# Kernel optimization log

Measured on AMD Instinct MI355X. Metric: run time of the kernel, lower is better.

## Reference

```python
import jax, jax.numpy as jnp
import numpy as np

EPS = 1e-5

def _ln(x, g, b):
    m = jnp.mean(x, axis=-1, keepdims=True)
    v = jnp.var(x, axis=-1, keepdims=True)
    return (x - m) / jnp.sqrt(v + EPS) * g + b

def _partition(x, nw):
    b, h, w, c = x.shape
    x = x.reshape(b, nw, h // nw, nw, w // nw, c).transpose(0, 1, 3, 2, 4, 5)
    return x.reshape(b * nw * nw, h // nw, w // nw, c)

def _merge(x, nw):
    b_, h, w, c = x.shape
    b = b_ // (nw * nw)
    x = x.reshape(b, nw, nw, h, w, c).transpose(0, 1, 3, 2, 4, 5)
    return x.reshape(b, nw * h, nw * w, c)

def _window_attn(q, k, v, width, height, nw, mask):
    b, _, c = q.shape
    q = q.reshape(b, height, width, c)
    k = k.reshape(b, height, width, c)
    v = v.reshape(b, height, width, c)
    sh, sw = (height // nw) // 2, (width // nw) // 2
    q = jnp.roll(q, (-sh, -sw), (1, 2))
    k = jnp.roll(k, (-sh, -sw), (1, 2))
    v = jnp.roll(v, (-sh, -sw), (1, 2))
    q = _partition(q, nw); k = _partition(k, nw); v = _partition(v, nw)
    N = (height // nw) * (width // nw)
    b_ = b * nw * nw
    qf = q.reshape(b_, N, c); kf = k.reshape(b_, N, c); vf = v.reshape(b_, N, c)
    scale = jnp.asarray(c, qf.dtype) ** 0.5
    scores = jnp.einsum('bnc,bmc->bnm', qf, kf) / scale  # [b_, N, N]
    scores = (scores.reshape(b, nw * nw, N, N) + mask[None]).reshape(b_, N, N)
    attn = jax.nn.softmax(scores, axis=-1)
    out = jnp.einsum('bnm,bmc->bnc', attn, vf)
    out = _merge(out.reshape(b_, height // nw, width // nw, c), nw)
    out = jnp.roll(out, (sh, sw), (1, 2))
    return out.reshape(b, height * width, c)

def _block(feat0, feat1, width, height, mask, nw, wq, wk, wv, wfc, g, be, ffn=None):
    q = feat0 @ wq; k = feat1 @ wk; v = feat1 @ wv
    a = _window_attn(q, k, v, width, height, nw, mask)
    a = _ln(a @ wfc, g, be)
    if ffn is not None:
        w1, w2, fg, fb = ffn
        h = jax.nn.gelu(jnp.concatenate([feat0, a], axis=-1) @ w1, approximate=False)
        a = _ln(h @ w2, fg, fb)
    return feat0 + a

def setup_inputs() -> dict:
    key = jax.random.key(0)
    B, H, W, NW, D = 8, 128, 128, 8, 256
    N = (H // NW) * (W // NW)
    ks = jax.random.split(key, 16)
    s = D ** -0.5
    return {
        'feat0': jax.random.normal(ks[0], (B, H * W, D), jnp.float32),
        'feat1': jax.random.normal(ks[1], (B, H * W, D), jnp.float32),
        'mask_attn': jax.random.normal(ks[2], (NW * NW, N, N), jnp.float32),
        'width': W, 'height': H, 'n_window': NW,
        'intra_wq': jax.random.normal(ks[3], (D, D), jnp.float32) * s,
        'intra_wk': jax.random.normal(ks[4], (D, D), jnp.float32) * s,
        'intra_wv': jax.random.normal(ks[5], (D, D), jnp.float32) * s,
        'intra_wfc': jax.random.normal(ks[6], (D, D), jnp.float32) * s,
        'intra_g': jnp.ones((D,), jnp.float32),
        'intra_b': jnp.zeros((D,), jnp.float32),
        'inter_wq': jax.random.normal(ks[7], (D, D), jnp.float32) * s,
        'inter_wk': jax.random.normal(ks[8], (D, D), jnp.float32) * s,
        'inter_wv': jax.random.normal(ks[9], (D, D), jnp.float32) * s,
        'inter_wfc': jax.random.normal(ks[10], (D, D), jnp.float32) * s,
        'inter_g': jnp.ones((D,), jnp.float32),
        'inter_b': jnp.zeros((D,), jnp.float32),
        'inter_w1': jax.random.normal(ks[11], (2 * D, 2 * D * 4), jnp.float32) * (2 * D) ** -0.5,
        'inter_w2': jax.random.normal(ks[12], (2 * D * 4, D), jnp.float32) * (2 * D * 4) ** -0.5,
        'inter_fg': jnp.ones((D,), jnp.float32),
        'inter_fb': jnp.zeros((D,), jnp.float32),
    }

def reference(feat0, feat1, mask_attn, width, height, n_window,
              intra_wq, intra_wk, intra_wv, intra_wfc, intra_g, intra_b,
              inter_wq, inter_wk, inter_wv, inter_wfc, inter_g, inter_b,
              inter_w1, inter_w2, inter_fg, inter_fb):
    f0 = _block(feat0, feat0, width, height, mask_attn, n_window,
                intra_wq, intra_wk, intra_wv, intra_wfc, intra_g, intra_b)
    out = _block(f0, feat1, width, height, mask_attn, n_window,
                 inter_wq, inter_wk, inter_wv, inter_wfc, inter_g, inter_b,
                 ffn=(inter_w1, inter_w2, inter_fg, inter_fb))
    return out
```

## Files before the change

### kernel.cpp

```cpp
#include <hip/hip_runtime.h>

typedef unsigned short u16;
typedef unsigned int   u32;

using f32x4  = __attribute__((ext_vector_type(4))) float;
using bf16x8 = __attribute__((ext_vector_type(8))) __bf16;

__device__ inline u16 f2bf(float f) {
  return __builtin_bit_cast(u16, (__bf16)f);
}
__device__ inline float bf2f(u16 v) {
  u32 u = ((u32)v) << 16;
  return __builtin_bit_cast(float, u);
}

__device__ inline void gl_lds16(const u16* g, u16* l) {
  __builtin_amdgcn_global_load_lds((const __attribute__((address_space(1))) void*)g,
                                   (__attribute__((address_space(3))) void*)l,
                                   16, 0, 0);
}

__device__ inline int perm_fwd(int m) {
  int b = m >> 14, rem = m & 16383;
  int h = rem >> 7, w = rem & 127;
  int hr = (h - 8) & 127, wr = (w - 8) & 127;
  int win = (b << 6) | ((hr >> 4) << 3) | (wr >> 4);
  return (win << 8) | ((hr & 15) << 4) | (wr & 15);
}
__device__ inline int perm_inv(int r) {
  int win = r >> 8, t = r & 255;
  int b = win >> 6, wy = (win >> 3) & 7, wx = win & 7;
  int h = (((wy << 4) | (t >> 4)) + 8) & 127;
  int w = (((wx << 4) | (t & 15)) + 8) & 127;
  return (b << 14) | (h << 7) | w;
}


enum { MODE_QKV = 0, MODE_SCORES = 1, MODE_PV = 2, MODE_F32 = 3, MODE_FFN1 = 4 };

template<int MODE>
__global__ __launch_bounds__(256)
void gemm_nt(const u16* __restrict__ A, int lda, long long sAz,
             const u16* __restrict__ Bt, int ldb, long long sBz,
             u16* __restrict__ OutB, float* __restrict__ OutF,
             const float* __restrict__ mask, int K, int ldo)
{
  __shared__ __align__(16) u16 sA[128 * 64];
  __shared__ __align__(16) u16 sB[128 * 64];

  const int tid  = threadIdx.x;
  const int lane = tid & 63;
  const int wave = tid >> 6;
  const int l15  = lane & 15;
  const int quad = lane >> 4;
  const int wm   = (wave >> 1) << 6;
  const int wn   = (wave & 1) << 6;
  const int z    = blockIdx.z;
  const int m0   = (int)(blockIdx.y) << 7;
  const int n0   = (int)(blockIdx.x) << 7;

  const u16* Ab = A  + (long long)z * sAz;
  const u16* Bb = Bt + (long long)z * sBz;

  const int cd = ((lane & 7) ^ ((lane >> 3) & 7)) << 3;
  const int rs = (wave << 5) + (lane >> 3);
  const u16* ga0 = Ab + (long long)(m0 + rs) * lda + cd;
  const u16* gb0 = Bb + (long long)(n0 + rs) * ldb + cd;
  u16* la0 = &sA[wave << 11];
  u16* lb0 = &sB[wave << 11];

  const f32x4 zero = {0.f, 0.f, 0.f, 0.f};
  f32x4 acc[4][4];
#pragma unroll
  for (int i = 0; i < 4; ++i)
#pragma unroll
    for (int j = 0; j < 4; ++j) acc[i][j] = zero;

  for (int k0 = 0; k0 < K; k0 += 64) {
    __syncthreads();
#pragma unroll
    for (int p = 0; p < 4; ++p) {
      gl_lds16(ga0 + k0 + (p << 3) * lda, la0 + (p << 9));
      gl_lds16(gb0 + k0 + (p << 3) * ldb, lb0 + (p << 9));
    }
    __syncthreads();
#pragma unroll
    for (int kk = 0; kk < 2; ++kk) {
      const int sw = (((quad | (kk << 2)) ^ (l15 & 7)) << 3);
      bf16x8 af[4], bfr[4];
#pragma unroll
      for (int i = 0; i < 4; ++i) {
        af[i]  = *(const bf16x8*)(sA + ((wm + (i << 4) + l15) << 6) + sw);
        bfr[i] = *(const bf16x8*)(sB + ((wn + (i << 4) + l15) << 6) + sw);
      }
#pragma unroll
      for (int i = 0; i < 4; ++i)
#pragma unroll
        for (int j = 0; j < 4; ++j)
          acc[i][j] = __builtin_amdgcn_mfma_f32_16x16x32_bf16(af[i], bfr[j], acc[i][j], 0, 0, 0);
    }
  }

#pragma unroll
  for (int i = 0; i < 4; ++i) {
#pragma unroll
    for (int r = 0; r < 4; ++r) {
      int mg = m0 + wm + (i << 4) + (quad << 2) + r;
      if constexpr (MODE == MODE_QKV) {
        u16* orow = OutB + ((long long)perm_fwd(mg) << 8);
#pragma unroll
        for (int j = 0; j < 4; ++j) {
          int ng = n0 + wn + (j << 4) + l15;
          orow[ng] = f2bf(acc[i][j][r]);
        }
      } else if constexpr (MODE == MODE_SCORES) {
        const float* mrow = mask + (((long long)(z & 63)) << 16) + ((long long)mg << 8);
        u16* orow = OutB + (((long long)z) << 16) + ((long long)mg << 8);
#pragma unroll
        for (int j = 0; j < 4; ++j) {
          int ng = n0 + wn + (j << 4) + l15;
          orow[ng] = f2bf(acc[i][j][r] * 0.0625f + mrow[ng]);
        }
      } else if constexpr (MODE == MODE_PV) {
        u16* orow = OutB + ((long long)perm_inv((z << 8) + mg) << 8);
#pragma unroll
        for (int j = 0; j < 4; ++j) {
          int ng = n0 + wn + (j << 4) + l15;
          orow[ng] = f2bf(acc[i][j][r]);
        }
      } else if constexpr (MODE == MODE_F32) {
        float* orow = OutF + ((long long)mg << 8);
#pragma unroll
        for (int j = 0; j < 4; ++j) {
          int ng = n0 + wn + (j << 4) + l15;
          orow[ng] = acc[i][j][r];
        }
      } else {
        u16* orow = OutB + (long long)mg * ldo;
#pragma unroll
        for (int j = 0; j < 4; ++j) {
          int ng = n0 + wn + (j << 4) + l15;
          float v = acc[i][j][r];
          float t = v * fmaf(v * v, -0.071354816f, -1.5957691216f);
          float g = v * __builtin_amdgcn_rcpf(1.0f + __expf(t));
          orow[ng] = f2bf(g);
        }
      }
    }
  }
}

__global__ __launch_bounds__(256)
void transpose256(const u16* __restrict__ src, u16* __restrict__ dst)
{
  __shared__ u16 t[32][33];
  const int z  = blockIdx.z;
  const int tx = blockIdx.x << 5;
  const int ty = blockIdx.y << 5;
  const int c  = threadIdx.x & 31;
  const int r0 = threadIdx.x >> 5;
  const long long base = ((long long)z) << 16;
#pragma unroll
  for (int p = 0; p < 4; ++p) {
    int r = r0 + (p << 3);
    t[r][c] = src[base + (long long)(ty + r) * 256 + tx + c];
  }
  __syncthreads();
#pragma unroll
  for (int p = 0; p < 4; ++p) {
    int r = r0 + (p << 3);
    dst[base + (long long)(tx + r) * 256 + ty + c] = t[c][r];
  }
}

__global__ __launch_bounds__(256)
void softmax_rows(u16* __restrict__ SP)
{
  const int row  = (blockIdx.x << 2) + (threadIdx.x >> 6);
  const int lane = threadIdx.x & 63;
  u16* rp = SP + ((long long)row << 8);
  ushort4 u = *((const ushort4*)rp + lane);
  float x0 = bf2f(u.x), x1 = bf2f(u.y), x2 = bf2f(u.z), x3 = bf2f(u.w);
  float mx = fmaxf(fmaxf(x0, x1), fmaxf(x2, x3));
#pragma unroll
  for (int o = 32; o > 0; o >>= 1) mx = fmaxf(mx, __shfl_xor(mx, o));
  float e0 = __expf(x0 - mx), e1 = __expf(x1 - mx), e2 = __expf(x2 - mx), e3 = __expf(x3 - mx);
  float s = e0 + e1 + e2 + e3;
#pragma unroll
  for (int o = 32; o > 0; o >>= 1) s += __shfl_xor(s, o);
  float inv = 1.0f / s;
  ushort4 o4;
  o4.x = f2bf(e0 * inv); o4.y = f2bf(e1 * inv); o4.z = f2bf(e2 * inv); o4.w = f2bf(e3 * inv);
  *((ushort4*)rp + lane) = o4;
}

template<int MODE>
__global__ __launch_bounds__(256)
void ln_kernel(const float* __restrict__ Y, const float* __restrict__ G,
               const float* __restrict__ Bb, const float* __restrict__ ResF,
               const u16* __restrict__ ResB,
               float* __restrict__ OutF, u16* __restrict__ OutB)
{
  const int row  = (blockIdx.x << 2) + (threadIdx.x >> 6);
  const int lane = threadIdx.x & 63;
  float4 x = *((const float4*)(Y + ((long long)row << 8)) + lane);
  float s  = x.x + x.y + x.z + x.w;
  float s2 = x.x * x.x + x.y * x.y + x.z * x.z + x.w * x.w;
#pragma unroll
  for (int o = 32; o > 0; o >>= 1) { s += __shfl_xor(s, o); s2 += __shfl_xor(s2, o); }
  float mean = s * (1.0f / 256.0f);
  float var  = s2 * (1.0f / 256.0f) - mean * mean;
  float rstd = rsqrtf(var + 1e-5f);
  float4 g = *((const float4*)G + lane);
  float4 b = *((const float4*)Bb + lane);
  float v0 = (x.x - mean) * rstd * g.x + b.x;
  float v1 = (x.y - mean) * rstd * g.y + b.y;
  float v2 = (x.z - mean) * rstd * g.z + b.z;
  float v3 = (x.w - mean) * rstd * g.w + b.w;
  if constexpr (MODE == 0) {
    float4 rr = *((const float4*)(ResF + ((long long)row << 8)) + lane);
    ushort4 ub;
    ub.x = f2bf(v0 + rr.x); ub.y = f2bf(v1 + rr.y);
    ub.z = f2bf(v2 + rr.z); ub.w = f2bf(v3 + rr.w);
    *((ushort4*)(OutB + ((long long)row << 9)) + lane) = ub;
  } else if constexpr (MODE == 1) {
    ushort4 ub; ub.x = f2bf(v0); ub.y = f2bf(v1); ub.z = f2bf(v2); ub.w = f2bf(v3);
    *((ushort4*)(OutB + ((long long)row << 9) + 256) + lane) = ub;
  } else {
    ushort4 rb = *((const ushort4*)(ResB + ((long long)row << 9)) + lane);
    float4 o;
    o.x = v0 + bf2f(rb.x); o.y = v1 + bf2f(rb.y);
    o.z = v2 + bf2f(rb.z); o.w = v3 + bf2f(rb.w);
    *((float4*)(OutF + ((long long)row << 8)) + lane) = o;
  }
}

__global__ __launch_bounds__(256)
void cvt_f32_bf16(const float* __restrict__ src, u16* __restrict__ dst, int n4)
{
  int i = blockIdx.x * 256 + threadIdx.x;
  if (i >= n4) return;
  float4 v = ((const float4*)src)[i];
  ushort4 u; u.x = f2bf(v.x); u.y = f2bf(v.y); u.z = f2bf(v.z); u.w = f2bf(v.w);
  ((ushort4*)dst)[i] = u;
}

__global__ __launch_bounds__(256)
void wtrans(const float* __restrict__ src, u16* __restrict__ dst, int R, int C)
{
  int idx = blockIdx.x * 256 + threadIdx.x;
  if (idx >= R * C) return;
  int r = idx / C, c = idx - r * C;
  dst[c * R + r] = f2bf(src[idx]);
}

extern "C" void kernel_launch(void* const* d_in, const int* in_sizes, int n_in,
                              void* d_out, int out_size, void* d_ws, size_t ws_size,
                              hipStream_t stream)
{
  (void)in_sizes; (void)n_in; (void)out_size;
  const float* feat0 = (const float*)d_in[0];
  const float* feat1 = (const float*)d_in[1];
  const float* mask  = (const float*)d_in[2];
  const float* wq1 = (const float*)d_in[6];
  const float* wk1 = (const float*)d_in[7];
  const float* wv1 = (const float*)d_in[8];
  const float* wf1 = (const float*)d_in[9];
  const float* g1  = (const float*)d_in[10];
  const float* b1  = (const float*)d_in[11];
  const float* wq2 = (const float*)d_in[12];
  const float* wk2 = (const float*)d_in[13];
  const float* wv2 = (const float*)d_in[14];
  const float* wf2 = (const float*)d_in[15];
  const float* g2  = (const float*)d_in[16];
  const float* b2  = (const float*)d_in[17];
  const float* w1  = (const float*)d_in[18];
  const float* w2  = (const float*)d_in[19];
  const float* fg  = (const float*)d_in[20];
  const float* fb  = (const float*)d_in[21];

  const size_t Mi = 1048576;
  const size_t WB = 4 * Mi;
  const int Mtot = 131072;

  int nc = 8;
  for (int c = 1; c <= 8; c <<= 1) {
    size_t S = (size_t)(Mtot / c) * 512;
    if (7 * S + WB <= ws_size) { nc = c; break; }
  }
  const int Mc = Mtot / nc;
  const size_t S = (size_t)Mc * 512;

  char* ws = (char*)d_ws;
  u16*   featb = (u16*)(ws);
  u16*   SPb   = featb;
  u16*   qw    = (u16*)(ws + S);
  u16*   Ob    = qw;
  u16*   hbuf  = featb;
  u16*   kw    = (u16*)(ws + 2 * S);
  u16*   vw    = (u16*)(ws + 3 * S);
  float* y     = (float*)(ws + 2 * S);
  u16*   vt    = (u16*)(ws + 4 * S);
  u16*   xcat  = (u16*)(ws + 5 * S);
  u16*   wb    = (u16*)(ws + 7 * S);
  u16* wq1t = wb;            u16* wk1t = wb + 65536;  u16* wv1t = wb + 131072; u16* wf1t = wb + 196608;
  u16* wq2t = wb + 262144;   u16* wk2t = wb + 327680; u16* wv2t = wb + 393216; u16* wf2t = wb + 458752;
  u16* w1t  = wb + 524288;
  u16* w2t  = wb + 524288 + 1048576;

  const dim3 blk(256);
  const dim3 gBig(2, Mc / 128, 1);
  const int  Wc = Mc / 256;
  const dim3 gWin(2, 2, Wc);
  const dim3 gTr(8, 8, Wc);
  const int  gRows = Mc / 4;
  const int  MF = Mc / 4;
  const dim3 gF1(16, MF / 128, 1);
  const dim3 gF2(2, MF / 128, 1);
  const int  gRowsF = MF / 4;

  wtrans<<<256, blk, 0, stream>>>(wq1, wq1t, 256, 256);
  wtrans<<<256, blk, 0, stream>>>(wk1, wk1t, 256, 256);
  wtrans<<<256, blk, 0, stream>>>(wv1, wv1t, 256, 256);
  wtrans<<<256, blk, 0, stream>>>(wf1, wf1t, 256, 256);
  wtrans<<<256, blk, 0, stream>>>(wq2, wq2t, 256, 256);
  wtrans<<<256, blk, 0, stream>>>(wk2, wk2t, 256, 256);
  wtrans<<<256, blk, 0, stream>>>(wv2, wv2t, 256, 256);
  wtrans<<<256, blk, 0, stream>>>(wf2, wf2t, 256, 256);
  wtrans<<<4096, blk, 0, stream>>>(w1, w1t, 512, 2048);
  wtrans<<<2048, blk, 0, stream>>>(w2, w2t, 2048, 256);

  for (int c = 0; c < nc; ++c) {
    const long long off = (long long)c * Mc * 256;
    const float* f0in = feat0 + off;
    const float* f1in = feat1 + off;
    float* outp = (float*)d_out + off;

    cvt_f32_bf16<<<gRows, blk, 0, stream>>>(f0in, featb, Mc * 64);
    gemm_nt<MODE_QKV><<<gBig, blk, 0, stream>>>(featb, 256, 0, wq1t, 256, 0, qw, nullptr, nullptr, 256, 0);
    gemm_nt<MODE_QKV><<<gBig, blk, 0, stream>>>(featb, 256, 0, wk1t, 256, 0, kw, nullptr, nullptr, 256, 0);
    gemm_nt<MODE_QKV><<<gBig, blk, 0, stream>>>(featb, 256, 0, wv1t, 256, 0, vw, nullptr, nullptr, 256, 0);
    transpose256<<<gTr, blk, 0, stream>>>(vw, vt);
    gemm_nt<MODE_SCORES><<<gWin, blk, 0, stream>>>(qw, 256, 65536, kw, 256, 65536, SPb, nullptr, mask, 256, 0);
    softmax_rows<<<gRows, blk, 0, stream>>>(SPb);
    gemm_nt<MODE_PV><<<gWin, blk, 0, stream>>>(SPb, 256, 65536, vt, 256, 65536, Ob, nullptr, nullptr, 256, 0);
    gemm_nt<MODE_F32><<<gBig, blk, 0, stream>>>(Ob, 256, 0, wf1t, 256, 0, nullptr, y, nullptr, 256, 0);
    ln_kernel<0><<<gRows, blk, 0, stream>>>(y, g1, b1, f0in, nullptr, nullptr, xcat);

    cvt_f32_bf16<<<gRows, blk, 0, stream>>>(f1in, featb, Mc * 64);
    gemm_nt<MODE_QKV><<<gBig, blk, 0, stream>>>(xcat, 512, 0, wq2t, 256, 0, qw, nullptr, nullptr, 256, 0);
    gemm_nt<MODE_QKV><<<gBig, blk, 0, stream>>>(featb, 256, 0, wk2t, 256, 0, kw, nullptr, nullptr, 256, 0);
    gemm_nt<MODE_QKV><<<gBig, blk, 0, stream>>>(featb, 256, 0, wv2t, 256, 0, vw, nullptr, nullptr, 256, 0);
    transpose256<<<gTr, blk, 0, stream>>>(vw, vt);
    gemm_nt<MODE_SCORES><<<gWin, blk, 0, stream>>>(qw, 256, 65536, kw, 256, 65536, SPb, nullptr, mask, 256, 0);
    softmax_rows<<<gRows, blk, 0, stream>>>(SPb);
    gemm_nt<MODE_PV><<<gWin, blk, 0, stream>>>(SPb, 256, 65536, vt, 256, 65536, Ob, nullptr, nullptr, 256, 0);
    gemm_nt<MODE_F32><<<gBig, blk, 0, stream>>>(Ob, 256, 0, wf2t, 256, 0, nullptr, y, nullptr, 256, 0);
    ln_kernel<1><<<gRows, blk, 0, stream>>>(y, g2, b2, nullptr, nullptr, nullptr, xcat);

    for (int mc = 0; mc < 4; ++mc) {
      const u16* xc = xcat + (long long)mc * MF * 512;
      gemm_nt<MODE_FFN1><<<gF1, blk, 0, stream>>>(xc, 512, 0, w1t, 512, 0,
                                                  hbuf, nullptr, nullptr, 512, 2048);
      gemm_nt<MODE_F32><<<gF2, blk, 0, stream>>>(hbuf, 2048, 0, w2t, 2048, 0,
                                                 nullptr, y, nullptr, 2048, 0);
      ln_kernel<2><<<gRowsF, blk, 0, stream>>>(y, fg, fb, nullptr,
                                               xcat + (long long)mc * MF * 512,
                                               outp + (long long)mc * MF * 256, nullptr);
    }
  }
}
```

Baseline: 1.858 ms.

## Fuse window scores GEMM with masked softmax and remap GEMM block order

Adds a scores_softmax kernel in which each block computes a 128x256 slab of window scores, so every row is held entirely in registers. It then applies scale and mask and runs softmax in place before writing bf16 probabilities, replacing the separate scores GEMM plus softmax_rows pass. This removes one write and re-read of the score matrix and one launch per block. Separately, gemm_nt now remaps block IDs in strides of 8, likely to spread neighbouring tiles across XCDs for better cache locality. The fused kernel holds 32 accumulators per thread and uses larger LDS, which may lower occupancy.

```diff
diff --git a/kernel.cpp b/kernel.cpp
--- a/kernel.cpp
+++ b/kernel.cpp
@@ -55,9 +55,17 @@
   const int quad = lane >> 4;
   const int wm   = (wave >> 1) << 6;
   const int wn   = (wave & 1) << 6;
-  const int z    = blockIdx.z;
-  const int m0   = (int)(blockIdx.y) << 7;
-  const int n0   = (int)(blockIdx.x) << 7;
+
+  const int nbx = (int)gridDim.x, nby = (int)gridDim.y;
+  const int nwg = nbx * nby * (int)gridDim.z;
+  const int bid0 = (int)blockIdx.x + nbx * ((int)blockIdx.y + nby * (int)blockIdx.z);
+  const int work = (bid0 & 7) * (nwg >> 3) + (bid0 >> 3);
+  const int bx  = work % nbx;
+  const int tm  = work / nbx;
+  const int by  = tm % nby;
+  const int z   = tm / nby;
+  const int m0  = by << 7;
+  const int n0  = bx << 7;
 
   const u16* Ab = A  + (long long)z * sAz;
   const u16* Bb = Bt + (long long)z * sBz;
@@ -151,6 +159,96 @@
 }
 
 __global__ __launch_bounds__(256)
+void scores_softmax(const u16* __restrict__ Q, const u16* __restrict__ Kw,
+                    const float* __restrict__ mask, u16* __restrict__ SP)
+{
+  __shared__ __align__(16) u16 sA[128 * 64];
+  __shared__ __align__(16) u16 sB[256 * 64];
+
+  const int tid  = threadIdx.x;
+  const int lane = tid & 63;
+  const int wave = tid >> 6;
+  const int l15  = lane & 15;
+  const int quad = lane >> 4;
+
+  const int nwg  = (int)(gridDim.x * gridDim.y);
+  const int bid0 = (int)blockIdx.x + (int)gridDim.x * (int)blockIdx.y;
+  const int work = (bid0 & 7) * (nwg >> 3) + (bid0 >> 3);
+  const int mhalf = work & 1;
+  const int z     = work >> 1;
+  const int m0    = mhalf << 7;
+
+  const u16* Ab = Q  + ((long long)z << 16);
+  const u16* Bb = Kw + ((long long)z << 16);
+
+  const int cd  = ((lane & 7) ^ ((lane >> 3) & 7)) << 3;
+  const int rsA = (wave << 5) + (lane >> 3);
+  const int rsB = (wave << 6) + (lane >> 3);
+  const u16* ga0 = Ab + (long long)(m0 + rsA) * 256 + cd;
+  const u16* gb0 = Bb + (long long)rsB * 256 + cd;
+  u16* la0 = &sA[wave << 11];
+  u16* lb0 = &sB[wave << 12];
+
+  const f32x4 zero = {0.f, 0.f, 0.f, 0.f};
+  f32x4 acc[2][16];
+#pragma unroll
+  for (int i = 0; i < 2; ++i)
+#pragma unroll
+    for (int j = 0; j < 16; ++j) acc[i][j] = zero;
+
+  for (int k0 = 0; k0 < 256; k0 += 64) {
+    __syncthreads();
+#pragma unroll
+    for (int p = 0; p < 4; ++p)
+      gl_lds16(ga0 + k0 + (p << 3) * 256, la0 + (p << 9));
+#pragma unroll
+    for (int p = 0; p < 8; ++p)
+      gl_lds16(gb0 + k0 + (p << 3) * 256, lb0 + (p << 9));
+    __syncthreads();
+#pragma unroll
+    for (int kk = 0; kk < 2; ++kk) {
+      const int sw = (((quad | (kk << 2)) ^ (l15 & 7)) << 3);
+      bf16x8 af0 = *(const bf16x8*)(sA + (((wave << 5) + l15) << 6) + sw);
+      bf16x8 af1 = *(const bf16x8*)(sA + (((wave << 5) + 16 + l15) << 6) + sw);
+#pragma unroll
+      for (int j = 0; j < 16; ++j) {
+        bf16x8 bf = *(const bf16x8*)(sB + (((j << 4) + l15) << 6) + sw);
+        acc[0][j] = __builtin_amdgcn_mfma_f32_16x16x32_bf16(af0, bf, acc[0][j], 0, 0, 0);
+        acc[1][j] = __builtin_amdgcn_mfma_f32_16x16x32_bf16(af1, bf, acc[1][j], 0, 0, 0);
+      }
+    }
+  }
+
+  const float* mbase = mask + (((long long)(z & 63)) << 16);
+#pragma unroll
+  for (int i = 0; i < 2; ++i) {
+#pragma unroll
+    for (int r = 0; r < 4; ++r) {
+      const int mg = m0 + (wave << 5) + (i << 4) + (quad << 2) + r;
+      const float* mrow = mbase + ((long long)mg << 8);
+      float sv[16];
+      float mx = -3.0e38f;
+#pragma unroll
+      for (int j = 0; j < 16; ++j) {
+        sv[j] = acc[i][j][r] * 0.0625f + mrow[(j << 4) + l15];
+        mx = fmaxf(mx, sv[j]);
+      }
+#pragma unroll
+      for (int o = 1; o < 16; o <<= 1) mx = fmaxf(mx, __shfl_xor(mx, o));
+      float sum = 0.f;
+#pragma unroll
+      for (int j = 0; j < 16; ++j) { sv[j] = __expf(sv[j] - mx); sum += sv[j]; }
+#pragma unroll
+      for (int o = 1; o < 16; o <<= 1) sum += __shfl_xor(sum, o);
+      const float inv = 1.0f / sum;
+      u16* orow = SP + (((long long)z) << 16) + ((long long)mg << 8);
+#pragma unroll
+      for (int j = 0; j < 16; ++j) orow[(j << 4) + l15] = f2bf(sv[j] * inv);
+    }
+  }
+}
+
+__global__ __launch_bounds__(256)
 void transpose256(const u16* __restrict__ src, u16* __restrict__ dst)
 {
   __shared__ u16 t[32][33];
@@ -171,27 +269,6 @@
     int r = r0 + (p << 3);
     dst[base + (long long)(tx + r) * 256 + ty + c] = t[c][r];
   }
-}
-
-__global__ __launch_bounds__(256)
-void softmax_rows(u16* __restrict__ SP)
-{
-  const int row  = (blockIdx.x << 2) + (threadIdx.x >> 6);
-  const int lane = threadIdx.x & 63;
-  u16* rp = SP + ((long long)row << 8);
-  ushort4 u = *((const ushort4*)rp + lane);
-  float x0 = bf2f(u.x), x1 = bf2f(u.y), x2 = bf2f(u.z), x3 = bf2f(u.w);
-  float mx = fmaxf(fmaxf(x0, x1), fmaxf(x2, x3));
-#pragma unroll
-  for (int o = 32; o > 0; o >>= 1) mx = fmaxf(mx, __shfl_xor(mx, o));
-  float e0 = __expf(x0 - mx), e1 = __expf(x1 - mx), e2 = __expf(x2 - mx), e3 = __expf(x3 - mx);
-  float s = e0 + e1 + e2 + e3;
-#pragma unroll
-  for (int o = 32; o > 0; o >>= 1) s += __shfl_xor(s, o);
-  float inv = 1.0f / s;
-  ushort4 o4;
-  o4.x = f2bf(e0 * inv); o4.y = f2bf(e1 * inv); o4.z = f2bf(e2 * inv); o4.w = f2bf(e3 * inv);
-  *((ushort4*)rp + lane) = o4;
 }
 
 template<int MODE>
@@ -312,6 +389,7 @@
   const dim3 gBig(2, Mc / 128, 1);
   const int  Wc = Mc / 256;
   const dim3 gWin(2, 2, Wc);
+  const dim3 gSS(2, Wc);
   const dim3 gTr(8, 8, Wc);
   const int  gRows = Mc / 4;
   const int  MF = Mc / 4;
@@ -341,8 +419,7 @@
     gemm_nt<MODE_QKV><<<gBig, blk, 0, stream>>>(featb, 256, 0, wk1t, 256, 0, kw, nullptr, nullptr, 256, 0);
     gemm_nt<MODE_QKV><<<gBig, blk, 0, stream>>>(featb, 256, 0, wv1t, 256, 0, vw, nullptr, nullptr, 256, 0);
     transpose256<<<gTr, blk, 0, stream>>>(vw, vt);
-    gemm_nt<MODE_SCORES><<<gWin, blk, 0, stream>>>(qw, 256, 65536, kw, 256, 65536, SPb, nullptr, mask, 256, 0);
-    softmax_rows<<<gRows, blk, 0, stream>>>(SPb);
+    scores_softmax<<<gSS, blk, 0, stream>>>(qw, kw, mask, SPb);
     gemm_nt<MODE_PV><<<gWin, blk, 0, stream>>>(SPb, 256, 65536, vt, 256, 65536, Ob, nullptr, nullptr, 256, 0);
     gemm_nt<MODE_F32><<<gBig, blk, 0, stream>>>(Ob, 256, 0, wf1t, 256, 0, nullptr, y, nullptr, 256, 0);
     ln_kernel<0><<<gRows, blk, 0, stream>>>(y, g1, b1, f0in, nullptr, nullptr, xcat);
@@ -352,8 +429,7 @@
     gemm_nt<MODE_QKV><<<gBig, blk, 0, stream>>>(featb, 256, 0, wk2t, 256, 0, kw, nullptr, nullptr, 256, 0);
     gemm_nt<MODE_QKV><<<gBig, blk, 0, stream>>>(featb, 256, 0, wv2t, 256, 0, vw, nullptr, nullptr, 256, 0);
     transpose256<<<gTr, blk, 0, stream>>>(vw, vt);
-    gemm_nt<MODE_SCORES><<<gWin, blk, 0, stream>>>(qw, 256, 65536, kw, 256, 65536, SPb, nullptr, mask, 256, 0);
-    softmax_rows<<<gRows, blk, 0, stream>>>(SPb);
+    scores_softmax<<<gSS, blk, 0, stream>>>(qw, kw, mask, SPb);
     gemm_nt<MODE_PV><<<gWin, blk, 0, stream>>>(SPb, 256, 65536, vt, 256, 65536, Ob, nullptr, nullptr, 256, 0);
     gemm_nt<MODE_F32><<<gBig, blk, 0, stream>>>(Ob, 256, 0, wf2t, 256, 0, nullptr, y, nullptr, 256, 0);
     ln_kernel<1><<<gRows, blk, 0, stream>>>(y, g2, b2, nullptr, nullptr, nullptr, xcat);
```

New measurement: 1.800 ms. 1.03x faster.
